# Performance work log

Measured on AMD Instinct MI355X. Metric: run time of the kernel, lower is better.

The kernel has to match this reference:

```python
import jax, jax.numpy as jnp
import numpy as np

# ---- static config (matches init_kwargs cfg) ----
N_IMGS, C_FEAT = 9, 24
HF, WF = 112, 112            # quarter-res feature map
H_IMG, W_IMG = 448, 448      # CDR.IMG_SIZE
HD, WD = 56, 56              # DEPTH_PRED_SIZE
N_PLANES = 64                # DEPTH_MVS.N_INTERVALS
DEPTH_START, DEPTH_INTERVAL = 0.5, 0.05
EDGES_PER_REF = 8
N_EDGES = N_IMGS * EDGES_PER_REF
N_PIX = HD * WD


def setup_inputs() -> dict:
    key = jax.random.key(0)
    k1, k2, k3, k4 = jax.random.split(key, 4)
    feats_quarter = jax.random.normal(k1, (N_IMGS, C_FEAT, HF, WF), jnp.float32)
    # proper rotation matrices via QR so the camera math is well conditioned
    A = jax.random.normal(k2, (N_IMGS, 3, 3), jnp.float32)
    rotmats, _ = jnp.linalg.qr(A)
    rotmats = rotmats.astype(jnp.float32)
    tvecs = 0.1 * jax.random.normal(k3, (N_IMGS, 3), jnp.float32)
    K = jnp.broadcast_to(
        jnp.array([[400.0, 0.0, (W_IMG - 1) / 2.0],
                   [0.0, 400.0, (H_IMG - 1) / 2.0],
                   [0.0, 0.0, 1.0]], jnp.float32), (N_IMGS, 3, 3))
    # ref index sorted+repeated so unique(return_inverse) == ref row itself
    ref = jnp.repeat(jnp.arange(N_IMGS, dtype=jnp.int32), EDGES_PER_REF)
    src = jax.random.randint(k4, (N_EDGES,), 0, N_IMGS, dtype=jnp.int32)
    ref_src_edges = jnp.stack([ref, src], 0)
    return {"feats_quarter": feats_quarter, "rotmats": rotmats,
            "tvecs": tvecs, "K": K, "ref_src_edges": ref_src_edges}


def _forward(feats_quarter, rotmats, tvecs, K, ref_src_edges):
    ref_e, src_e = ref_src_edges[0], ref_src_edges[1]

    # ---- batched_build_plane_sweep_volume_tensor: world-space points per ref view ----
    us = jnp.linspace(0.0, W_IMG - 1.0, WD)
    vs = jnp.linspace(0.0, H_IMG - 1.0, HD)
    uu, vv = jnp.meshgrid(us, vs)                              # [HD, WD]
    pix = jnp.stack([uu, vv, jnp.ones_like(uu)], 0).reshape(3, N_PIX)
    rays = jnp.einsum('nij,jp->nip', jnp.linalg.inv(K), pix)  # [N, 3, P]
    depths = DEPTH_START + DEPTH_INTERVAL * jnp.arange(N_PLANES, dtype=jnp.float32)
    pts_cam = rays[:, None] * depths[None, :, None, None]      # [N, D, 3, P] (plane-major)
    pts_cam = pts_cam.transpose(0, 2, 1, 3).reshape(N_IMGS, 3, N_PLANES * N_PIX)
    pts_world = jnp.einsum('nji,njp->nip', rotmats, pts_cam - tvecs[:, :, None])
    n_pts = N_PLANES * N_PIX

    # ---- project ref-volume points into each src view (per edge) ----
    pts_homo = jnp.concatenate([pts_world, jnp.ones((N_IMGS, 1, n_pts), jnp.float32)], 1)
    P = jnp.einsum('nij,njk->nik', K, jnp.concatenate([rotmats, tvecs[:, :, None]], 2))  # [N,3,4]
    proj = jnp.einsum('eij,ejp->eip', P[src_e], pts_homo[ref_e])  # [E, 3, n_pts]
    z = jnp.abs(proj[:, 2]) + 1e-8
    gx = proj[:, 0] / z / (W_IMG - 1.0) * 2.0 - 1.0
    gy = proj[:, 1] / z / (H_IMG - 1.0) * 2.0 - 1.0

    # ---- bilinear grid_sample, align_corners=True, zeros padding ----
    def sample_one(img, gx1, gy1):  # img [C,HF,WF], gx1/gy1 [n_pts]
        x = (gx1 + 1.0) * 0.5 * (WF - 1)
        y = (gy1 + 1.0) * 0.5 * (HF - 1)
        x0 = jnp.floor(x)
        y0 = jnp.floor(y)
        wx1 = x - x0
        wy1 = y - y0

        def tap(xi, yi, w):
            valid = (xi >= 0) & (xi <= WF - 1) & (yi >= 0) & (yi <= HF - 1)
            xc = jnp.clip(xi, 0, WF - 1).astype(jnp.int32)
            yc = jnp.clip(yi, 0, HF - 1).astype(jnp.int32)
            return jnp.where(valid, w, 0.0)[None] * img[:, yc, xc]  # [C, n_pts]

        return (tap(x0, y0, (1 - wx1) * (1 - wy1))
                + tap(x0 + 1, y0, wx1 * (1 - wy1))
                + tap(x0, y0 + 1, (1 - wx1) * wy1)
                + tap(x0 + 1, y0 + 1, wx1 * wy1))

    x_vox = jax.vmap(sample_one)(feats_quarter[src_e], gx, gy)   # [E, C, n_pts]
    x_vox = x_vox.reshape(N_EDGES, C_FEAT, N_PLANES, HD, WD)

    # ---- scatter mean / sq-mean over edges sharing a ref image, then variance ----
    counts = jax.ops.segment_sum(jnp.ones((N_EDGES,), jnp.float32), ref_e, num_segments=N_IMGS)
    denom = jnp.maximum(counts, 1.0)[:, None, None, None, None]
    x_avg = jax.ops.segment_sum(x_vox, ref_e, num_segments=N_IMGS) / denom
    x_avg_sq = jax.ops.segment_sum(x_vox ** 2, ref_e, num_segments=N_IMGS) / denom
    return x_avg_sq - x_avg ** 2  # [n_ref, C, D, HD, WD]


def reference(feats_quarter, rotmats, tvecs, K, ref_src_edges):
    return _forward(feats_quarter, rotmats, tvecs, K, ref_src_edges)
```

## Files before the change

### kernel.cpp

```cpp
#include <hip/hip_runtime.h>

constexpr int kNImgs   = 9;
constexpr int kC       = 24;
constexpr int kHF      = 112, kWF = 112;
constexpr int kHD      = 56,  kWD = 56;
constexpr int kNPix    = kHD * kWD;
constexpr int kNPlanes = 64;
constexpr int kPtsPerRef = kNPlanes * kNPix;
constexpr int kEdgesPerRef = 8;
constexpr int kNEdges  = kNImgs * kEdgesPerRef;
constexpr int kFeatPix = kHF * kWF;
constexpr int kFeatPerImg = kC * kFeatPix;

typedef _Float16 half8 __attribute__((ext_vector_type(8)));

__device__ inline void mm3(const float* A, const float* B, float* C) {
#pragma unroll
  for (int i = 0; i < 3; ++i)
#pragma unroll
    for (int j = 0; j < 3; ++j)
      C[i*3+j] = A[i*3+0]*B[0*3+j] + A[i*3+1]*B[1*3+j] + A[i*3+2]*B[2*3+j];
}

__device__ inline void inv3(const float* A, float* I) {
  float a=A[0],b=A[1],c=A[2],d=A[3],e=A[4],f=A[5],g=A[6],h=A[7],i=A[8];
  float c00 = e*i - f*h;
  float c01 = -(d*i - f*g);
  float c02 = d*h - e*g;
  float det = a*c00 + b*c01 + c*c02;
  float r = 1.0f / det;
  I[0] = c00*r;           I[1] = (c*h - b*i)*r;  I[2] = (b*f - c*e)*r;
  I[3] = c01*r;           I[4] = (a*i - c*g)*r;  I[5] = (c*d - a*f)*r;
  I[6] = c02*r;           I[7] = (b*g - a*h)*r;  I[8] = (a*e - b*d)*r;
}

__global__ __launch_bounds__(256)
void transpose_feats_kernel(const float* __restrict__ f, _Float16* __restrict__ ft) {
  int idx = blockIdx.x * 256 + threadIdx.x;
  if (idx >= kNImgs * kFeatPerImg) return;
  int n  = idx / kFeatPerImg;
  int r  = idx - n * kFeatPerImg;
  int c  = r / kFeatPix;
  int yx = r - c * kFeatPix;
  ft[((size_t)n * kFeatPix + yx) * kC + c] = (_Float16)f[idx];
}

template <bool TR>
__global__ __launch_bounds__(256)
void psv_var_kernel(const float* __restrict__ feats,
                    const _Float16* __restrict__ featsT,
                    const float* __restrict__ rotmats,
                    const float* __restrict__ tvecs,
                    const float* __restrict__ Kmat,
                    const int*   __restrict__ edges,
                    float* __restrict__ out) {
  __shared__ float sM[kEdgesPerRef][9];
  __shared__ float sB[kEdgesPerRef][3];
  __shared__ int   sSrc[kEdgesPerRef];
  __shared__ int   sUIdx[kEdgesPerRef];
  __shared__ float sMult[kEdgesPerRef];
  __shared__ int   sKU;

  const int nwg = gridDim.x;
  int bid = blockIdx.x;
  if ((nwg & 7) == 0) {
    const int cpx = nwg >> 3;
    bid = (bid & 7) * cpx + (bid >> 3);
  }

  const int tid = bid * 256 + threadIdx.x;
  const int n = tid / kPtsPerRef;

  if (threadIdx.x < kEdgesPerRef) {
    const int e  = n * kEdgesPerRef + threadIdx.x;
    const int re = edges[e];
    const int se = edges[kNEdges + e];
    sSrc[threadIdx.x] = se;

    const float* Rr = rotmats + re * 9;
    const float* Rs = rotmats + se * 9;
    const float* Kr = Kmat + re * 9;
    const float* Ks = Kmat + se * 9;
    const float* tr = tvecs + re * 3;
    const float* ts = tvecs + se * 3;

    float RrT[9];
#pragma unroll
    for (int i = 0; i < 3; ++i)
#pragma unroll
      for (int j = 0; j < 3; ++j) RrT[i*3+j] = Rr[j*3+i];

    float Kinv[9], A[9], T1[9], M[9];
    inv3(Kr, Kinv);
    mm3(Rs, RrT, A);
    mm3(A, Kinv, T1);
    mm3(Ks, T1, M);

    float At0 = A[0]*tr[0] + A[1]*tr[1] + A[2]*tr[2];
    float At1 = A[3]*tr[0] + A[4]*tr[1] + A[5]*tr[2];
    float At2 = A[6]*tr[0] + A[7]*tr[1] + A[8]*tr[2];
    float bv0 = ts[0] - At0, bv1 = ts[1] - At1, bv2 = ts[2] - At2;
#pragma unroll
    for (int i = 0; i < 9; ++i) sM[threadIdx.x][i] = M[i];
#pragma unroll
    for (int i = 0; i < 3; ++i)
      sB[threadIdx.x][i] = Ks[i*3+0]*bv0 + Ks[i*3+1]*bv1 + Ks[i*3+2]*bv2;
  }
  __syncthreads();

  if (threadIdx.x == 0) {
    int k = 0;
    for (int j = 0; j < kEdgesPerRef; ++j) {
      const int s = sSrc[j];
      bool dup = false;
      for (int i = 0; i < k; ++i) {
        if (sSrc[sUIdx[i]] == s) { sMult[i] += 1.0f; dup = true; break; }
      }
      if (!dup) { sUIdx[k] = j; sMult[k] = 1.0f; ++k; }
    }
    sKU = k;
  }
  __syncthreads();

  const int local = tid - n * kPtsPerRef;
  const int d = local / kNPix;
  const int p = local - d * kNPix;
  const int h = p / kWD;
  const int w = p - h * kWD;

  const float u = (float)w * (447.0f / 55.0f);
  const float v = (float)h * (447.0f / 55.0f);
  const float depth = 0.5f + 0.05f * (float)d;

  float acc[kC], accsq[kC];
#pragma unroll
  for (int c = 0; c < kC; ++c) { acc[c] = 0.0f; accsq[c] = 0.0f; }

  const int kU = sKU;
#pragma unroll 2
  for (int jj = 0; jj < kU; ++jj) {
    const int j = sUIdx[jj];
    const float mult = sMult[jj];
    const float* M = sM[j];
    const float px = depth * (M[0]*u + M[1]*v + M[2]) + sB[j][0];
    const float py = depth * (M[3]*u + M[4]*v + M[5]) + sB[j][1];
    const float pz = depth * (M[6]*u + M[7]*v + M[8]) + sB[j][2];
    const float rz = 1.0f / (fabsf(pz) + 1e-8f);

    const float x = px * rz * (111.0f / 447.0f);
    const float y = py * rz * (111.0f / 447.0f);

    const float x0 = floorf(x), y0 = floorf(y);
    const float wx = x - x0, wy = y - y0;
    const bool vx0 = (x0 >= 0.0f)  && (x0 <= 111.0f);
    const bool vx1 = (x0 >= -1.0f) && (x0 <= 110.0f);
    const bool vy0 = (y0 >= 0.0f)  && (y0 <= 111.0f);
    const bool vy1 = (y0 >= -1.0f) && (y0 <= 110.0f);
    const float w00 = (vx0 && vy0) ? (1.0f - wx) * (1.0f - wy) : 0.0f;
    const float w01 = (vx1 && vy0) ? wx * (1.0f - wy) : 0.0f;
    const float w10 = (vx0 && vy1) ? (1.0f - wx) * wy : 0.0f;
    const float w11 = (vx1 && vy1) ? wx * wy : 0.0f;

    const int xc0 = (int)fminf(fmaxf(x0,        0.0f), 111.0f);
    const int xc1 = (int)fminf(fmaxf(x0 + 1.0f, 0.0f), 111.0f);
    const int yc0 = (int)fminf(fmaxf(y0,        0.0f), 111.0f);
    const int yc1 = (int)fminf(fmaxf(y0 + 1.0f, 0.0f), 111.0f);

    const int src = sSrc[j];
    if constexpr (TR) {
      const _Float16* base = featsT + (size_t)src * kFeatPix * kC;
      const int o00 = (yc0 * kWF + xc0) * kC;
      const int o01 = (yc0 * kWF + xc1) * kC;
      const int o10 = (yc1 * kWF + xc0) * kC;
      const int o11 = (yc1 * kWF + xc1) * kC;
#pragma unroll
      for (int i = 0; i < kC / 8; ++i) {
        const half8 f00 = *(const half8*)(base + o00 + 8*i);
        const half8 f01 = *(const half8*)(base + o01 + 8*i);
        const half8 f10 = *(const half8*)(base + o10 + 8*i);
        const half8 f11 = *(const half8*)(base + o11 + 8*i);
#pragma unroll
        for (int k = 0; k < 8; ++k) {
          float val = w00 * (float)f00[k] + w01 * (float)f01[k]
                    + w10 * (float)f10[k] + w11 * (float)f11[k];
          const int c = 8*i + k;
          const float mval = mult * val;
          acc[c] += mval;
          accsq[c] = __builtin_fmaf(mval, val, accsq[c]);
        }
      }
    } else {
      const float* base = feats + (size_t)src * kFeatPerImg;
      const int o00 = yc0 * kWF + xc0;
      const int o01 = yc0 * kWF + xc1;
      const int o10 = yc1 * kWF + xc0;
      const int o11 = yc1 * kWF + xc1;
#pragma unroll
      for (int c = 0; c < kC; ++c) {
        const float* bc = base + c * kFeatPix;
        float val = w00*bc[o00] + w01*bc[o01] + w10*bc[o10] + w11*bc[o11];
        const float mval = mult * val;
        acc[c] += mval;
        accsq[c] = __builtin_fmaf(mval, val, accsq[c]);
      }
    }
  }

  float* op = out + ((size_t)n * kC * kNPlanes + d) * kNPix + p;
#pragma unroll
  for (int c = 0; c < kC; ++c) {
    float mean = acc[c] * 0.125f;
    float msq  = accsq[c] * 0.125f;
    op[(size_t)c * (kNPlanes * kNPix)] = msq - mean * mean;
  }
}

extern "C" void kernel_launch(void* const* d_in, const int* in_sizes, int n_in,
                              void* d_out, int out_size, void* d_ws, size_t ws_size,
                              hipStream_t stream) {
  const float* feats  = (const float*)d_in[0];
  const float* rot    = (const float*)d_in[1];
  const float* tv     = (const float*)d_in[2];
  const float* Kmat   = (const float*)d_in[3];
  const int*   edges  = (const int*)d_in[4];
  float* out = (float*)d_out;

  const size_t featsTBytes = (size_t)kNImgs * kFeatPix * kC * sizeof(_Float16);
  const int nMain = kNImgs * kPtsPerRef;
  const int gridMain = nMain / 256;

  if (ws_size >= featsTBytes) {
    _Float16* featsT = (_Float16*)d_ws;
    const int nT = kNImgs * kFeatPerImg;
    transpose_feats_kernel<<<(nT + 255) / 256, 256, 0, stream>>>(feats, featsT);
    psv_var_kernel<true><<<gridMain, 256, 0, stream>>>(feats, featsT, rot, tv, Kmat, edges, out);
  } else {
    psv_var_kernel<false><<<gridMain, 256, 0, stream>>>(feats, nullptr, rot, tv, Kmat, edges, out);
  }
}
```

Baseline: 184.8 us.

## Tile main kernel as 32 depth x 32 pixel blocks with LDS-transposed output

```diff
diff --git a/kernel.cpp b/kernel.cpp
--- a/kernel.cpp
+++ b/kernel.cpp
@@ -12,6 +12,11 @@
 constexpr int kFeatPix = kHF * kWF;
 constexpr int kFeatPerImg = kC * kFeatPix;
 
+constexpr int kDTile = 32, kPTile = 32;
+constexpr int kDHalves = kNPlanes / kDTile;
+constexpr int kPGroups = kNPix / kPTile;
+constexpr int kBlocksPerRef = kDHalves * kPGroups;
+
 typedef _Float16 half8 __attribute__((ext_vector_type(8)));
 
 __device__ inline void mm3(const float* A, const float* B, float* C) {
@@ -46,7 +51,7 @@
 }
 
 template <bool TR>
-__global__ __launch_bounds__(256)
+__global__ __launch_bounds__(1024, 4)
 void psv_var_kernel(const float* __restrict__ feats,
                     const _Float16* __restrict__ featsT,
                     const float* __restrict__ rotmats,
@@ -60,22 +65,26 @@
   __shared__ int   sUIdx[kEdgesPerRef];
   __shared__ float sMult[kEdgesPerRef];
   __shared__ int   sKU;
+  __shared__ float sT[4][kDTile][kPTile + 1];
 
   const int nwg = gridDim.x;
-  int bid = blockIdx.x;
-  if ((nwg & 7) == 0) {
-    const int cpx = nwg >> 3;
-    bid = (bid & 7) * cpx + (bid >> 3);
-  }
-
-  const int tid = bid * 256 + threadIdx.x;
-  const int n = tid / kPtsPerRef;
-
-  if (threadIdx.x < kEdgesPerRef) {
-    const int e  = n * kEdgesPerRef + threadIdx.x;
+  const int orig = blockIdx.x;
+  const int q = nwg >> 3, r8 = nwg & 7;
+  const int xcd = orig & 7, lin = orig >> 3;
+  const int bid = ((xcd < r8) ? xcd * (q + 1) : r8 * (q + 1) + (xcd - r8) * q) + lin;
+
+  const int n     = bid / kBlocksPerRef;
+  const int rem   = bid - n * kBlocksPerRef;
+  const int dHalf = rem / kPGroups;
+  const int pG    = rem - dHalf * kPGroups;
+
+  const int t = threadIdx.x;
+
+  if (t < kEdgesPerRef) {
+    const int e  = n * kEdgesPerRef + t;
     const int re = edges[e];
     const int se = edges[kNEdges + e];
-    sSrc[threadIdx.x] = se;
+    sSrc[t] = se;
 
     const float* Rr = rotmats + re * 9;
     const float* Rs = rotmats + se * 9;
@@ -101,14 +110,14 @@
     float At2 = A[6]*tr[0] + A[7]*tr[1] + A[8]*tr[2];
     float bv0 = ts[0] - At0, bv1 = ts[1] - At1, bv2 = ts[2] - At2;
 #pragma unroll
-    for (int i = 0; i < 9; ++i) sM[threadIdx.x][i] = M[i];
+    for (int i = 0; i < 9; ++i) sM[t][i] = M[i];
 #pragma unroll
     for (int i = 0; i < 3; ++i)
-      sB[threadIdx.x][i] = Ks[i*3+0]*bv0 + Ks[i*3+1]*bv1 + Ks[i*3+2]*bv2;
+      sB[t][i] = Ks[i*3+0]*bv0 + Ks[i*3+1]*bv1 + Ks[i*3+2]*bv2;
   }
   __syncthreads();
 
-  if (threadIdx.x == 0) {
+  if (t == 0) {
     int k = 0;
     for (int j = 0; j < kEdgesPerRef; ++j) {
       const int s = sSrc[j];
@@ -122,9 +131,10 @@
   }
   __syncthreads();
 
-  const int local = tid - n * kPtsPerRef;
-  const int d = local / kNPix;
-  const int p = local - d * kNPix;
+  const int dsub = t & 31;
+  const int psub = t >> 5;
+  const int d = dHalf * kDTile + dsub;
+  const int p = pG * kPTile + psub;
   const int h = p / kWD;
   const int w = p - h * kWD;
 
@@ -206,12 +216,26 @@
     }
   }
 
-  float* op = out + ((size_t)n * kC * kNPlanes + d) * kNPix + p;
-#pragma unroll
-  for (int c = 0; c < kC; ++c) {
-    float mean = acc[c] * 0.125f;
-    float msq  = accsq[c] * 0.125f;
-    op[(size_t)c * (kNPlanes * kNPix)] = msq - mean * mean;
+  const int pp2 = t & 31;
+  const int dd2 = t >> 5;
+  const size_t outBase = (size_t)n * kC * (size_t)kPtsPerRef;
+#pragma unroll
+  for (int ch = 0; ch < kC / 4; ++ch) {
+    __syncthreads();
+#pragma unroll
+    for (int cc = 0; cc < 4; ++cc) {
+      const int c = ch * 4 + cc;
+      const float mean = acc[c] * 0.125f;
+      const float msq  = accsq[c] * 0.125f;
+      sT[cc][dsub][psub] = msq - mean * mean;
+    }
+    __syncthreads();
+#pragma unroll
+    for (int cc = 0; cc < 4; ++cc) {
+      const int c = ch * 4 + cc;
+      out[outBase + ((size_t)c * kNPlanes + (dHalf * kDTile + dd2)) * kNPix
+          + pG * kPTile + pp2] = sT[cc][dd2][pp2];
+    }
   }
 }
 
@@ -226,15 +250,14 @@
   float* out = (float*)d_out;
 
   const size_t featsTBytes = (size_t)kNImgs * kFeatPix * kC * sizeof(_Float16);
-  const int nMain = kNImgs * kPtsPerRef;
-  const int gridMain = nMain / 256;
+  const int gridMain = kNImgs * kBlocksPerRef;
 
   if (ws_size >= featsTBytes) {
     _Float16* featsT = (_Float16*)d_ws;
     const int nT = kNImgs * kFeatPerImg;
     transpose_feats_kernel<<<(nT + 255) / 256, 256, 0, stream>>>(feats, featsT);
-    psv_var_kernel<true><<<gridMain, 256, 0, stream>>>(feats, featsT, rot, tv, Kmat, edges, out);
+    psv_var_kernel<true><<<gridMain, 1024, 0, stream>>>(feats, featsT, rot, tv, Kmat, edges, out);
   } else {
-    psv_var_kernel<false><<<gridMain, 256, 0, stream>>>(feats, nullptr, rot, tv, Kmat, edges, out);
-  }
-}
+    psv_var_kernel<false><<<gridMain, 1024, 0, stream>>>(feats, nullptr, rot, tv, Kmat, edges, out);
+  }
+}
```

After: 171.2 us. 7.3% less time.
